# Performance work log

Hardware: AMD Instinct MI355X
Metric: run time of the kernel (lower is better)

The kernel has to match this reference:

```python
import jax, jax.numpy as jnp
import numpy as np

BS, SEQ, DK = 4, 4096, 128

def setup_inputs() -> dict:
    key = jax.random.key(0)
    kq, kk, kv = jax.random.split(key, 3)
    q = jax.random.normal(kq, (BS, SEQ, DK), dtype=jnp.float32)
    k = jax.random.normal(kk, (BS, SEQ, DK), dtype=jnp.float32)
    v = jax.random.normal(kv, (BS, SEQ, DK), dtype=jnp.float32)
    return {"q": q, "k": k, "v": v}

def reference(q, k, v):
    d_k = q.shape[-1]
    # scores: [bs, s_q, s_k]
    scaled = jnp.einsum('bqd,bkd->bqk', q, k) / jnp.sqrt(jnp.asarray(d_k, q.dtype))
    # NOTE: original torch code applies softmax over dim=1 (query axis), faithfully reproduced here.
    attn = jax.nn.softmax(scaled, axis=1)
    return jnp.einsum('bqk,bkd->bqd', attn, v)
```

## Files before the change

kernel.cpp:

```cpp
#include <hip/hip_runtime.h>
#include <hip/hip_bf16.h>

#define BS  4
#define SEQ 4096
#define DK  128

#define C1_SCALE (1.4426950408889634f / 11.313708498984761f)

typedef __attribute__((ext_vector_type(8))) short bf16x8;
typedef __attribute__((ext_vector_type(4))) float f32x4;
typedef unsigned short ushort_t;

__device__ inline unsigned pk_bf16(float a, float b) {
    __hip_bfloat162 h = __float22bfloat162_rn(make_float2(a, b));
    union { __hip_bfloat162 h2; unsigned u; } cv;
    cv.h2 = h;
    return cv.u;
}

__device__ inline bf16x8 pk8(float4 a, float4 b) {
    union { bf16x8 v; unsigned u[4]; } r;
    r.u[0] = pk_bf16(a.x, a.y);
    r.u[1] = pk_bf16(a.z, a.w);
    r.u[2] = pk_bf16(b.x, b.y);
    r.u[3] = pk_bf16(b.z, b.w);
    return r.v;
}

__device__ inline void gld_lds16(const ushort_t* g, ushort_t* l) {
    __builtin_amdgcn_global_load_lds(
        (const __attribute__((address_space(1))) unsigned int*)g,
        (__attribute__((address_space(3))) unsigned int*)l,
        16, 0, 0);
}

__device__ inline void bar_fence() {
    __builtin_amdgcn_s_barrier();
    asm volatile("" ::: "memory");
}

__global__ __launch_bounds__(256) void cast_qk_sw(
    const float* __restrict__ Q, const float* __restrict__ K,
    ushort_t* __restrict__ Qb, ushort_t* __restrict__ Kb)
{
    const int g = blockIdx.x * 256 + threadIdx.x;
    const int q = g >> 4, ap = g & 15;
    const int a = ap ^ (q & 15);
    const float* src = Q + (size_t)q * DK + a * 8;
    float4 x = *(const float4*)src, y = *(const float4*)(src + 4);
    x.x *= C1_SCALE; x.y *= C1_SCALE; x.z *= C1_SCALE; x.w *= C1_SCALE;
    y.x *= C1_SCALE; y.y *= C1_SCALE; y.z *= C1_SCALE; y.w *= C1_SCALE;
    *(bf16x8*)(Qb + (size_t)g * 8) = pk8(x, y);
    src = K + (size_t)q * DK + a * 8;
    float4 x2 = *(const float4*)src, y2 = *(const float4*)(src + 4);
    *(bf16x8*)(Kb + (size_t)g * 8) = pk8(x2, y2);
}

__global__ __launch_bounds__(256) void sdpa_passA(
    const ushort_t* __restrict__ Qb, const ushort_t* __restrict__ Kb,
    ushort_t* __restrict__ Pg, float* __restrict__ lp)
{
    __shared__ ushort_t Qs[3][4096];

    const int kt = blockIdx.x, qs = blockIdx.y, b = blockIdx.z;
    const int tid = threadIdx.x;
    const int w = tid >> 6, lane = tid & 63, ln = lane & 15, quad = lane >> 4;

    bf16x8 ka[2][4];
#pragma unroll
    for (int mt = 0; mt < 2; ++mt)
#pragma unroll
        for (int c = 0; c < 4; ++c)
            ka[mt][c] = *(const bf16x8*)(Kb +
                ((size_t)(b * SEQ) + kt * 128 + w * 32 + mt * 16 + ln) * DK +
                (((c * 4 + quad) ^ ln) * 8));

    float ls[2][4] = {};
    const ushort_t* qtb = Qb + ((size_t)(b * SEQ + qs * 512)) * DK;
    ushort_t* pgw = Pg + (((size_t)(b * 64 + qs * 8)) * 64 + kt * 2 + (w >> 1)) * 4096;

#define A_DMA(BUF, I)                                                          \
    {                                                                          \
        _Pragma("unroll")                                                      \
        for (int j = 0; j < 2; ++j)                                            \
            gld_lds16(qtb + (size_t)(I) * 4096 + (j * 256 + tid) * 8,          \
                      &Qs[BUF][(j * 256 + w * 64) * 8]);                       \
    }

#define A_CMP(BUF, T)                                                          \
    {                                                                          \
        bf16x8 qf[2][4];                                                       \
        _Pragma("unroll")                                                      \
        for (int nt = 0; nt < 2; ++nt)                                         \
            _Pragma("unroll")                                                  \
            for (int c = 0; c < 4; ++c)                                        \
                qf[nt][c] = *(const bf16x8*)&Qs[BUF][(nt * 16 + ln) * 128 +    \
                                    (((c * 4 + quad) ^ ln) * 8)];              \
        ushort_t* pgt = pgw + (size_t)((T) >> 1) * (64 * 4096);                \
        _Pragma("unroll")                                                      \
        for (int mt = 0; mt < 2; ++mt)                                         \
            _Pragma("unroll")                                                  \
            for (int nt = 0; nt < 2; ++nt) {                                   \
                f32x4 s = {0.f, 0.f, 0.f, 0.f};                                \
                __builtin_amdgcn_s_setprio(1);                                 \
                _Pragma("unroll")                                              \
                for (int c = 0; c < 4; ++c)                                    \
                    s = __builtin_amdgcn_mfma_f32_16x16x32_bf16(               \
                        ka[mt][c], qf[nt][c], s, 0, 0, 0);                     \
                __builtin_amdgcn_s_setprio(0);                                 \
                float e0 = __builtin_amdgcn_exp2f(s[0]);                       \
                float e1 = __builtin_amdgcn_exp2f(s[1]);                       \
                float e2 = __builtin_amdgcn_exp2f(s[2]);                       \
                float e3 = __builtin_amdgcn_exp2f(s[3]);                       \
                ls[mt][0] += e0; ls[mt][1] += e1;                              \
                ls[mt][2] += e2; ls[mt][3] += e3;                              \
                uint2 pw; pw.x = pk_bf16(e0, e1); pw.y = pk_bf16(e2, e3);      \
                const int ql = (((T) & 1) * 32) + nt * 16 + ln;                \
                const int aa = (w & 1) * 4 + mt * 2 + (quad >> 1);             \
                *(uint2*)&pgt[(ql * 8 + (aa ^ (ql & 7))) * 8 + (quad & 1) * 4] = pw; \
            }                                                                  \
    }

    A_DMA(0, 0)
    A_DMA(1, 1)
    for (int t = 0; t < 16; ++t) {
        if (t == 0)      asm volatile("s_waitcnt vmcnt(2)"  ::: "memory");
        else if (t == 1) asm volatile("s_waitcnt vmcnt(6)"  ::: "memory");
        else if (t < 15) asm volatile("s_waitcnt vmcnt(10)" ::: "memory");
        else             asm volatile("s_waitcnt vmcnt(8)"  ::: "memory");
        bar_fence();
        if (t < 14) A_DMA((t + 2) % 3, t + 2)
        A_CMP(t % 3, t)
    }
#undef A_DMA
#undef A_CMP

#pragma unroll
    for (int mt = 0; mt < 2; ++mt)
#pragma unroll
        for (int r = 0; r < 4; ++r) {
            float vv = ls[mt][r];
            vv += __shfl_xor(vv, 1);
            vv += __shfl_xor(vv, 2);
            vv += __shfl_xor(vv, 4);
            vv += __shfl_xor(vv, 8);
            ls[mt][r] = vv;
        }
    if (ln < 8) {
        int k = kt * 128 + w * 32 + (ln >> 2) * 16 + quad * 4 + (ln & 3);
        lp[((size_t)(qs * BS + b)) * SEQ + k] = ls[ln >> 2][ln & 3];
    }
}

__global__ __launch_bounds__(256) void vb_transpose(
    const float* __restrict__ V, const float* __restrict__ lp,
    ushort_t* __restrict__ VbT)
{
    __shared__ float Vl[64][132];
    __shared__ float Wl[64];

    const int kt = blockIdx.x, b = blockIdx.y;
    const int tid = threadIdx.x;
    const int k0 = kt * 64;
    {
        int r = tid >> 2, sg = tid & 3;
        const float* src = V + ((size_t)(b * SEQ) + k0 + r) * DK + sg * 32;
#pragma unroll
        for (int i = 0; i < 8; ++i)
            *(float4*)&Vl[r][sg * 32 + i * 4] = *(const float4*)(src + i * 4);
    }
    if (tid < 64) {
        float s = 0.f;
#pragma unroll
        for (int qs = 0; qs < 8; ++qs)
            s += lp[((size_t)(qs * BS + b)) * SEQ + k0 + tid];
        Wl[tid] = 1.0f / s;
    }
    __syncthreads();

    const int d = tid >> 1, kh = tid & 1;
    unsigned u[16];
#pragma unroll
    for (int j = 0; j < 16; ++j) {
        int row = kh * 32 + j * 2;
        u[j] = pk_bf16(Vl[row][d] * Wl[row], Vl[row + 1][d] * Wl[row + 1]);
    }
    ushort_t* dst = VbT + ((size_t)(b * DK) + d) * SEQ + k0 + kh * 32;
#pragma unroll
    for (int i = 0; i < 4; ++i) {
        uint4 t4; t4.x = u[i*4]; t4.y = u[i*4+1]; t4.z = u[i*4+2]; t4.w = u[i*4+3];
        *(uint4*)(dst + i * 8) = t4;
    }
}

__global__ __launch_bounds__(256) void sdpa_pv(
    const ushort_t* __restrict__ Pg, const ushort_t* __restrict__ VbT,
    float* __restrict__ O)
{
    __shared__ ushort_t Pt[3][2048];
    __shared__ ushort_t Vt[3][8192];

    const int qt32 = blockIdx.x, b = blockIdx.y;
    const int qt64 = qt32 >> 1, qh = qt32 & 1;
    const int tid = threadIdx.x;
    const int w = tid >> 6, lane = tid & 63, ln = lane & 15, quad = lane >> 4;
    const int vd = tid >> 3, vap = tid & 7;

    f32x4 acc[2][2];
#pragma unroll
    for (int i = 0; i < 2; ++i)
#pragma unroll
        for (int j = 0; j < 2; ++j) acc[i][j] = (f32x4){0.f, 0.f, 0.f, 0.f};

    const ushort_t* psrc = Pg + ((size_t)(b * 64 + qt64)) * 64 * 4096 + qh * 2048;
    const ushort_t* vsrc = VbT + ((size_t)(b * DK)) * SEQ;

#define B_DMA(BUF, T)                                                          \
    {                                                                          \
        gld_lds16(psrc + (size_t)(T) * 4096 + tid * 8,                         \
                  &Pt[BUF][(w * 64) * 8]);                                     \
        _Pragma("unroll")                                                      \
        for (int j = 0; j < 4; ++j)                                            \
            gld_lds16(vsrc + (size_t)(j * 32 + vd) * SEQ + (T) * 64 +          \
                          ((vap ^ (vd & 7)) * 8),                              \
                      &Vt[BUF][(j * 256 + w * 64) * 8]);                       \
    }

#define B_CMP(BUF)                                                             \
    {                                                                          \
        _Pragma("unroll")                                                      \
        for (int kc = 0; kc < 2; ++kc) {                                       \
            bf16x8 pa[2], vfr[2];                                              \
            _Pragma("unroll")                                                  \
            for (int qf2 = 0; qf2 < 2; ++qf2)                                  \
                pa[qf2] = *(const bf16x8*)&Pt[BUF][(qf2 * 16 + ln) * 64 +      \
                                    (((kc * 4 + quad) ^ (ln & 7)) * 8)];       \
            _Pragma("unroll")                                                  \
            for (int dt = 0; dt < 2; ++dt)                                     \
                vfr[dt] = *(const bf16x8*)&Vt[BUF][(w * 32 + dt * 16 + ln) * 64 + \
                                    (((kc * 4 + quad) ^ (ln & 7)) * 8)];       \
            __builtin_amdgcn_s_setprio(1);                                     \
            _Pragma("unroll")                                                  \
            for (int qf2 = 0; qf2 < 2; ++qf2)                                  \
                _Pragma("unroll")                                              \
                for (int dt = 0; dt < 2; ++dt)                                 \
                    acc[qf2][dt] = __builtin_amdgcn_mfma_f32_16x16x32_bf16(    \
                        pa[qf2], vfr[dt], acc[qf2][dt], 0, 0, 0);              \
            __builtin_amdgcn_s_setprio(0);                                     \
        }                                                                      \
    }

    B_DMA(0, 0)
    B_DMA(1, 1)
    for (int t = 0; t < 64; ++t) {
        if (t < 63) asm volatile("s_waitcnt vmcnt(5)" ::: "memory");
        else        asm volatile("s_waitcnt vmcnt(0)" ::: "memory");
        bar_fence();
        if (t < 62) B_DMA((t + 2) % 3, t + 2)
        B_CMP(t % 3)
    }
#undef B_DMA
#undef B_CMP

    float* dst = O + ((size_t)(b * SEQ) + qt32 * 32 + quad * 4) * DK + w * 32 + ln;
#pragma unroll
    for (int qf2 = 0; qf2 < 2; ++qf2)
#pragma unroll
        for (int dt = 0; dt < 2; ++dt)
#pragma unroll
            for (int r = 0; r < 4; ++r)
                dst[((size_t)(qf2 * 16 + r)) * DK + dt * 16] = acc[qf2][dt][r];
}

extern "C" void kernel_launch(void* const* d_in, const int* in_sizes, int n_in,
                              void* d_out, int out_size, void* d_ws, size_t ws_size,
                              hipStream_t stream) {
    const float* q = (const float*)d_in[0];
    const float* k = (const float*)d_in[1];
    const float* v = (const float*)d_in[2];
    float* out = (float*)d_out;

    const size_t QKV = (size_t)BS * SEQ * DK;
    float*    lp  = (float*)d_ws;
    ushort_t* Qb  = (ushort_t*)((char*)d_ws + (1 << 20));
    ushort_t* Kb  = Qb + QKV;
    ushort_t* VbT = Kb + QKV;
    ushort_t* Pg  = VbT + QKV;
    (void)ws_size;

    cast_qk_sw <<<dim3(BS * SEQ * 16 / 256), 256, 0, stream>>>(q, k, Qb, Kb);
    sdpa_passA <<<dim3(32, 8, 4), 256, 0, stream>>>(Qb, Kb, Pg, lp);
    vb_transpose<<<dim3(64, 4),   256, 0, stream>>>(v, lp, VbT);
    sdpa_pv    <<<dim3(128, 4),   256, 0, stream>>>(Pg, VbT, out);
}
```

Measured before the change: 155.1 us.

## Split PV kernel K-dimension across waves with per-wave buffers and LDS reduction

Restructures the PV kernel so each of the four waves owns a separate slice of the key dimension and its own LDS buffer. Each wave then computes the full 32x128 output tile for its slice, and the partial sums are reduced through LDS at the end. Each wave now waits only on its own loads, so the per-iteration block barrier is removed and the triple buffer becomes a double buffer. In exchange each wave holds more accumulators, which raises register pressure, and the final cross-wave reduction adds LDS traffic.

```diff
diff --git a/kernel.cpp b/kernel.cpp
--- a/kernel.cpp
+++ b/kernel.cpp
@@ -197,79 +197,95 @@
     const ushort_t* __restrict__ Pg, const ushort_t* __restrict__ VbT,
     float* __restrict__ O)
 {
-    __shared__ ushort_t Pt[3][2048];
-    __shared__ ushort_t Vt[3][8192];
+    __shared__ ushort_t S[2][4][5120];
 
     const int qt32 = blockIdx.x, b = blockIdx.y;
     const int qt64 = qt32 >> 1, qh = qt32 & 1;
     const int tid = threadIdx.x;
     const int w = tid >> 6, lane = tid & 63, ln = lane & 15, quad = lane >> 4;
-    const int vd = tid >> 3, vap = tid & 7;
-
-    f32x4 acc[2][2];
+    const int lr = lane >> 2, lp = lane & 3;
+
+    f32x4 acc[2][8];
 #pragma unroll
     for (int i = 0; i < 2; ++i)
 #pragma unroll
-        for (int j = 0; j < 2; ++j) acc[i][j] = (f32x4){0.f, 0.f, 0.f, 0.f};
-
-    const ushort_t* psrc = Pg + ((size_t)(b * 64 + qt64)) * 64 * 4096 + qh * 2048;
-    const ushort_t* vsrc = VbT + ((size_t)(b * DK)) * SEQ;
-
-#define B_DMA(BUF, T)                                                          \
+        for (int j = 0; j < 8; ++j) acc[i][j] = (f32x4){0.f, 0.f, 0.f, 0.f};
+
+    const ushort_t* ptile0 = Pg + (((size_t)(b * 64 + qt64)) * 64 + w * 16) * 4096
+                              + qh * 32 * 64;
+    const ushort_t* vbase  = VbT + ((size_t)(b * DK)) * SEQ + w * 1024;
+
+#define PV_DMA(BUF, T)                                                         \
     {                                                                          \
-        gld_lds16(psrc + (size_t)(T) * 4096 + tid * 8,                         \
-                  &Pt[BUF][(w * 64) * 8]);                                     \
-        _Pragma("unroll")                                                      \
-        for (int j = 0; j < 4; ++j)                                            \
-            gld_lds16(vsrc + (size_t)(j * 32 + vd) * SEQ + (T) * 64 +          \
-                          ((vap ^ (vd & 7)) * 8),                              \
-                      &Vt[BUF][(j * 256 + w * 64) * 8]);                       \
-    }
-
-#define B_CMP(BUF)                                                             \
+        const ushort_t* pt = ptile0 + (size_t)((T) >> 1) * 4096;               \
+        const int h4 = ((T) & 1) * 4;                                          \
+        _Pragma("unroll")                                                      \
+        for (int i = 0; i < 2; ++i) {                                          \
+            const int ql = i * 16 + lr;                                        \
+            gld_lds16(pt + ql * 64 + (((h4 + lp) ^ (ql & 7)) * 8),             \
+                      &S[BUF][w][i * 512]);                                    \
+        }                                                                      \
+        _Pragma("unroll")                                                      \
+        for (int j = 0; j < 8; ++j) {                                          \
+            const int d = j * 16 + lr;                                         \
+            gld_lds16(vbase + (size_t)d * SEQ + (T) * 32 + lp * 8,             \
+                      &S[BUF][w][1024 + j * 512]);                             \
+        }                                                                      \
+    }
+
+#define PV_CMP(BUF)                                                            \
     {                                                                          \
-        _Pragma("unroll")                                                      \
-        for (int kc = 0; kc < 2; ++kc) {                                       \
-            bf16x8 pa[2], vfr[2];                                              \
-            _Pragma("unroll")                                                  \
-            for (int qf2 = 0; qf2 < 2; ++qf2)                                  \
-                pa[qf2] = *(const bf16x8*)&Pt[BUF][(qf2 * 16 + ln) * 64 +      \
-                                    (((kc * 4 + quad) ^ (ln & 7)) * 8)];       \
-            _Pragma("unroll")                                                  \
-            for (int dt = 0; dt < 2; ++dt)                                     \
-                vfr[dt] = *(const bf16x8*)&Vt[BUF][(w * 32 + dt * 16 + ln) * 64 + \
-                                    (((kc * 4 + quad) ^ (ln & 7)) * 8)];       \
+        bf16x8 pa[2];                                                          \
+        _Pragma("unroll")                                                      \
+        for (int qf2 = 0; qf2 < 2; ++qf2)                                      \
+            pa[qf2] = *(const bf16x8*)&S[BUF][w][(qf2 * 16 + ln) * 32 + quad * 8]; \
+        _Pragma("unroll")                                                      \
+        for (int dt = 0; dt < 8; ++dt) {                                       \
+            bf16x8 vf = *(const bf16x8*)&S[BUF][w][1024 + (dt * 16 + ln) * 32 + quad * 8]; \
             __builtin_amdgcn_s_setprio(1);                                     \
-            _Pragma("unroll")                                                  \
-            for (int qf2 = 0; qf2 < 2; ++qf2)                                  \
-                _Pragma("unroll")                                              \
-                for (int dt = 0; dt < 2; ++dt)                                 \
-                    acc[qf2][dt] = __builtin_amdgcn_mfma_f32_16x16x32_bf16(    \
-                        pa[qf2], vfr[dt], acc[qf2][dt], 0, 0, 0);              \
+            acc[0][dt] = __builtin_amdgcn_mfma_f32_16x16x32_bf16(pa[0], vf, acc[0][dt], 0, 0, 0); \
+            acc[1][dt] = __builtin_amdgcn_mfma_f32_16x16x32_bf16(pa[1], vf, acc[1][dt], 0, 0, 0); \
             __builtin_amdgcn_s_setprio(0);                                     \
         }                                                                      \
     }
 
-    B_DMA(0, 0)
-    B_DMA(1, 1)
-    for (int t = 0; t < 64; ++t) {
-        if (t < 63) asm volatile("s_waitcnt vmcnt(5)" ::: "memory");
-        else        asm volatile("s_waitcnt vmcnt(0)" ::: "memory");
-        bar_fence();
-        if (t < 62) B_DMA((t + 2) % 3, t + 2)
-        B_CMP(t % 3)
-    }
-#undef B_DMA
-#undef B_CMP
-
-    float* dst = O + ((size_t)(b * SEQ) + qt32 * 32 + quad * 4) * DK + w * 32 + ln;
+    PV_DMA(0, 0)
+    PV_DMA(1, 1)
+    for (int t = 0; t < 32; ++t) {
+        if (t < 31) asm volatile("s_waitcnt vmcnt(10)" ::: "memory");
+        else        asm volatile("s_waitcnt vmcnt(0)"  ::: "memory");
+        PV_CMP(t & 1)
+        asm volatile("s_waitcnt lgkmcnt(0)" ::: "memory");
+        if (t < 30) PV_DMA(t & 1, t + 2)
+    }
+#undef PV_DMA
+#undef PV_CMP
+
+    float* R = (float*)&S[0][0][0];
+    __syncthreads();
 #pragma unroll
     for (int qf2 = 0; qf2 < 2; ++qf2)
 #pragma unroll
-        for (int dt = 0; dt < 2; ++dt)
+        for (int dt = 0; dt < 8; ++dt)
 #pragma unroll
             for (int r = 0; r < 4; ++r)
-                dst[((size_t)(qf2 * 16 + r)) * DK + dt * 16] = acc[qf2][dt][r];
+                R[w * 4352 + (qf2 * 16 + quad * 4 + r) * 136 + dt * 16 + ln] =
+                    acc[qf2][dt][r];
+    __syncthreads();
+    {
+        const int q = tid >> 3, d0 = (tid & 7) * 16;
+        float* dst = O + ((size_t)(b * SEQ) + qt32 * 32 + q) * DK + d0;
+#pragma unroll
+        for (int ii = 0; ii < 4; ++ii) {
+            float4 s4; s4.x = s4.y = s4.z = s4.w = 0.f;
+#pragma unroll
+            for (int wv = 0; wv < 4; ++wv) {
+                const float* r4 = &R[wv * 4352 + q * 136 + d0 + ii * 4];
+                s4.x += r4[0]; s4.y += r4[1]; s4.z += r4[2]; s4.w += r4[3];
+            }
+            *(float4*)(dst + ii * 4) = s4;
+        }
+    }
 }
 
 extern "C" void kernel_launch(void* const* d_in, const int* in_sizes, int n_in,
```

Result: slower. 159.9 us (+3.1%).
